# Kernel tuning notes

Measured on AMD Instinct MI355X. Metric: run time of the kernel, lower is better.

## Reference

```python
import jax, jax.numpy as jnp
import numpy as np

H = 16       # num_heads (groups for complex conv)
A = 32       # num frequency anchors
KSZ = 5      # complex conv kernel size
PAD = (KSZ - 1) // 2  # circular padding, matches ComplexConv1DLayer


def setup_inputs() -> dict:
    key = jax.random.key(0)
    ks = jax.random.split(key, 12)
    B, N, D = 4, 2048, 1024
    hid, ghid = 256, 256  # pooling MLP hidden, gate MLP hidden
    F = N // 2 + 1

    def rn(k, shp, s=0.02):
        return jax.random.normal(k, shp, jnp.float32) * s

    return {
        "x": jax.random.normal(ks[0], (B, N, D), jnp.float32),
        "Wv": rn(ks[1], (D, D)), "bv": jnp.zeros((D,), jnp.float32),
        "Wp1": rn(ks[2], (D, hid)), "bp1": jnp.zeros((hid,), jnp.float32),
        "Wp2": rn(ks[3], (hid, 1)), "bp2": jnp.zeros((1,), jnp.float32),
        "Wg1": rn(ks[4], (D, ghid)), "bg1": jnp.zeros((ghid,), jnp.float32),
        "Wg2": rn(ks[5], (ghid, 2 * H * A)), "bg2": jnp.zeros((2 * H * A,), jnp.float32),
        "mod_bias": jnp.zeros((F,), jnp.float32),
        "conv_kr": rn(ks[6], (KSZ,), 1.0 / np.sqrt(KSZ)),
        "conv_ki": rn(ks[7], (KSZ,), 1.0 / np.sqrt(KSZ)),
        "Wo": rn(ks[8], (D, D)), "bo": jnp.zeros((D,), jnp.float32),
    }


def reference(x, Wv, bv, Wp1, bp1, Wp2, bp2, Wg1, bg1, Wg2, bg2,
              mod_bias, conv_kr, conv_ki, Wo, bo):
    B, N, D = x.shape
    dh = D // H
    F = N // 2 + 1

    # value projection -> per-head sequences, rFFT over sequence axis
    v = (x @ Wv + bv).reshape(B, N, H, dh).transpose(0, 2, 1, 3)   # (B,H,N,dh)
    Vf = jnp.fft.rfft(v, axis=2)                                   # (B,H,F,dh) complex64

    # AttentionPoolingLayer: two-layer MLP scores -> softmax over seq -> weighted sum
    s = jax.nn.gelu(x @ Wp1 + bp1, approximate=False) @ Wp2 + bp2  # (B,N,1)
    w = jax.nn.softmax(s, axis=1)
    g = jnp.sum(x * w, axis=1)                                     # (B,D)

    # gate MLP -> complex anchors (B,H,A)
    a = (jax.nn.gelu(g @ Wg1 + bg1, approximate=False) @ Wg2 + bg2).reshape(B, H, A, 2)
    anch_r, anch_i = a[..., 0], a[..., 1]

    # ComplexInterpolationLayer: cubic interpolation of anchors to F bins
    gr = jax.image.resize(anch_r, (B, H, F), method="cubic")
    gi = jax.image.resize(anch_i, (B, H, F), method="cubic")
    gate = gr + 1j * gi                                            # (B,H,F)

    # ComplexModReLULayer: ReLU(|z|+b) * z / |z| with per-frequency bias
    mag = jnp.abs(gate)
    gate = gate * (jax.nn.relu(mag + mod_bias) / (mag + 1e-8))

    # ComplexConv1DLayer: circular-pad complex conv along frequency
    gp = jnp.concatenate([gate[..., -PAD:], gate, gate[..., :PAD]], axis=-1)
    ker = conv_kr.astype(jnp.complex64) + 1j * conv_ki.astype(jnp.complex64)
    gate = sum(ker[j] * gp[..., j:j + F] for j in range(KSZ))      # (B,H,F)

    # spectral gating + inverse FFT + output projection
    y = jnp.fft.irfft(Vf * gate[..., None], n=N, axis=2)           # (B,H,N,dh)
    y = y.transpose(0, 2, 1, 3).reshape(B, N, D)
    return y @ Wo + bo
```

## Files before the change

kernel.cpp:

```cpp
#include <hip/hip_runtime.h>
#include <math.h>

#define NSEQ 2048
#define DMOD 1024
#define NBATCH 4
#define NHEAD 16
#define NFREQ 1025

typedef unsigned short u16t;
typedef __attribute__((ext_vector_type(8))) short short8;
typedef __attribute__((ext_vector_type(4))) float f32x4;

__device__ __forceinline__ float gelu_exact(float x) {
  return 0.5f * x * (1.0f + erff(x * 0.70710678118654752440f));
}
__device__ __forceinline__ u16t bf16_rtn(float x) {
  unsigned u = __float_as_uint(x);
  return (u16t)((u + 0x7FFFu + ((u >> 16) & 1u)) >> 16);
}
__device__ __forceinline__ float bf16f(u16t h) {
  return __uint_as_float(((unsigned)h) << 16);
}
__device__ __forceinline__ void gload_lds16(const u16t* g, u16t* l) {
  __builtin_amdgcn_global_load_lds(
      (const __attribute__((address_space(1))) void*)g,
      (__attribute__((address_space(3))) void*)l, 16, 0, 0);
}

__global__ __launch_bounds__(256) void prep_kernel(
    const float* __restrict__ x, u16t* __restrict__ x_hi, u16t* __restrict__ x_lo,
    const float* __restrict__ Wv, u16t* __restrict__ Tvh, u16t* __restrict__ Tvl,
    const float* __restrict__ Wp1, u16t* __restrict__ Tph, u16t* __restrict__ Tpl) {
  __shared__ float tile[32][33];
  int bx = blockIdx.x;
  int tid = threadIdx.x;
  if (bx < 2048) {
    const int n8 = (NBATCH * NSEQ * DMOD) / 8;
    for (int i = bx * 256 + tid; i < n8; i += 2048 * 256) {
      const float4* p = reinterpret_cast<const float4*>(x + (size_t)i * 8);
      float4 a = p[0], b = p[1];
      float vv[8] = {a.x, a.y, a.z, a.w, b.x, b.y, b.z, b.w};
      alignas(16) u16t th[8];
      alignas(16) u16t tl[8];
#pragma unroll
      for (int e = 0; e < 8; ++e) {
        u16t h = bf16_rtn(vv[e]);
        th[e] = h;
        tl[e] = bf16_rtn(vv[e] - bf16f(h));
      }
      *reinterpret_cast<uint4*>(x_hi + (size_t)i * 8) = *reinterpret_cast<const uint4*>(th);
      *reinterpret_cast<uint4*>(x_lo + (size_t)i * 8) = *reinterpret_cast<const uint4*>(tl);
    }
  } else {
    int idx = bx - 2048;
    int wcol = idx % 40, k0 = (idx / 40) * 32;
    const float* W; u16t* Th; u16t* Tl; int N, n0;
    if (wcol < 32) { W = Wv;  Th = Tvh; Tl = Tvl; N = 1024; n0 = wcol * 32; }
    else           { W = Wp1; Th = Tph; Tl = Tpl; N = 256;  n0 = (wcol - 32) * 32; }
    const int K = 1024;
    int r = tid >> 5, c = tid & 31;
#pragma unroll
    for (int i = 0; i < 4; ++i)
      tile[r + 8 * i][c] = W[(size_t)(k0 + r + 8 * i) * N + n0 + c];
    __syncthreads();
#pragma unroll
    for (int i = 0; i < 4; ++i) {
      int rr = r + 8 * i;
      float v = tile[c][rr];
      u16t h = bf16_rtn(v);
      Th[(size_t)(n0 + rr) * K + k0 + c] = h;
      Tl[(size_t)(n0 + rr) * K + k0 + c] = bf16_rtn(v - bf16f(h));
    }
  }
}

__global__ __launch_bounds__(256) void gemm_fused_kernel(
    const u16t* __restrict__ Ah_g, const u16t* __restrict__ Al_g,
    const u16t* __restrict__ Bvh, const u16t* __restrict__ Bvl,
    const u16t* __restrict__ Bph, const u16t* __restrict__ Bpl,
    const float* __restrict__ bv, const float* __restrict__ bp1,
    const float* __restrict__ Wp2,
    float* __restrict__ vT, float* __restrict__ s_part) {
  __shared__ u16t Ahs[128 * 64], Als[128 * 64], Bhs[128 * 64], Bls[128 * 64];
  __shared__ u16t Php[32 * 64], Ppl[32 * 64];
  const int tid = threadIdx.x;
  const int lane = tid & 63, wave = tid >> 6;
  const int lr = lane & 15, lg = lane >> 4;
  const int wm0 = (wave >> 1) * 64, wn0 = (wave & 1) * 64;
  const int nwg = gridDim.x;
  const int L = (blockIdx.x & 7) * (nwg >> 3) + (blockIdx.x >> 3);
  const int m0 = (L >> 3) * 128;
  const int nblk = L & 7;
  const int n0 = nblk * 128;
  const int pc0 = nblk * 32;
  const int K = 1024;

  f32x4 acc[4][4];
#pragma unroll
  for (int i = 0; i < 4; ++i)
#pragma unroll
    for (int j = 0; j < 4; ++j) acc[i][j] = 0.0f;
  f32x4 accp[2][2];
#pragma unroll
  for (int i = 0; i < 2; ++i)
#pragma unroll
    for (int j = 0; j < 2; ++j) accp[i][j] = 0.0f;

  for (int k0 = 0; k0 < K; k0 += 64) {
#pragma unroll
    for (int q = 0; q < 4; ++q) {
      int cid = q * 256 + tid;
      int row = cid >> 3, grp = cid & 7;
      int koff = k0 + ((grp ^ (row & 7)) << 3);
      size_t ea = (size_t)(m0 + row) * K + koff;
      size_t eb = (size_t)(n0 + row) * K + koff;
      int lbase = q * 2048 + wave * 512;
      gload_lds16(Ah_g + ea, Ahs + lbase);
      gload_lds16(Al_g + ea, Als + lbase);
      gload_lds16(Bvh + eb, Bhs + lbase);
      gload_lds16(Bvl + eb, Bls + lbase);
    }
    {
      int row = tid >> 3, grp = tid & 7;
      int koff = k0 + ((grp ^ (row & 7)) << 3);
      size_t ep = (size_t)(pc0 + row) * K + koff;
      int lbase = wave * 512;
      gload_lds16(Bph + ep, Php + lbase);
      gload_lds16(Bpl + ep, Ppl + lbase);
    }
    __syncthreads();
#pragma unroll
    for (int kf = 0; kf < 2; ++kf) {
      short8 ah[4], al[4];
#pragma unroll
      for (int mi = 0; mi < 4; ++mi) {
        int r_ = wm0 + mi * 16 + lr;
        int g = (kf * 4 + lg) ^ (r_ & 7);
        ah[mi] = *reinterpret_cast<const short8*>(&Ahs[r_ * 64 + g * 8]);
        al[mi] = *reinterpret_cast<const short8*>(&Als[r_ * 64 + g * 8]);
      }
#pragma unroll
      for (int ni = 0; ni < 4; ++ni) {
        int r_ = wn0 + ni * 16 + lr;
        int g = (kf * 4 + lg) ^ (r_ & 7);
        short8 bh8 = *reinterpret_cast<const short8*>(&Bhs[r_ * 64 + g * 8]);
        short8 bl8 = *reinterpret_cast<const short8*>(&Bls[r_ * 64 + g * 8]);
#pragma unroll
        for (int mi = 0; mi < 4; ++mi) {
          acc[mi][ni] = __builtin_amdgcn_mfma_f32_16x16x32_bf16(ah[mi], bh8, acc[mi][ni], 0, 0, 0);
          acc[mi][ni] = __builtin_amdgcn_mfma_f32_16x16x32_bf16(ah[mi], bl8, acc[mi][ni], 0, 0, 0);
          acc[mi][ni] = __builtin_amdgcn_mfma_f32_16x16x32_bf16(al[mi], bh8, acc[mi][ni], 0, 0, 0);
        }
      }
      short8 pah[2], pal[2];
#pragma unroll
      for (int mi = 0; mi < 2; ++mi) {
        int r_ = wave * 32 + mi * 16 + lr;
        int g = (kf * 4 + lg) ^ (r_ & 7);
        pah[mi] = *reinterpret_cast<const short8*>(&Ahs[r_ * 64 + g * 8]);
        pal[mi] = *reinterpret_cast<const short8*>(&Als[r_ * 64 + g * 8]);
      }
#pragma unroll
      for (int ni = 0; ni < 2; ++ni) {
        int r_ = ni * 16 + lr;
        int g = (kf * 4 + lg) ^ (r_ & 7);
        short8 pbh = *reinterpret_cast<const short8*>(&Php[r_ * 64 + g * 8]);
        short8 pbl = *reinterpret_cast<const short8*>(&Ppl[r_ * 64 + g * 8]);
#pragma unroll
        for (int mi = 0; mi < 2; ++mi) {
          accp[mi][ni] = __builtin_amdgcn_mfma_f32_16x16x32_bf16(pah[mi], pbh, accp[mi][ni], 0, 0, 0);
          accp[mi][ni] = __builtin_amdgcn_mfma_f32_16x16x32_bf16(pah[mi], pbl, accp[mi][ni], 0, 0, 0);
          accp[mi][ni] = __builtin_amdgcn_mfma_f32_16x16x32_bf16(pal[mi], pbh, accp[mi][ni], 0, 0, 0);
        }
      }
    }
    __syncthreads();
  }
#pragma unroll
  for (int mi = 0; mi < 4; ++mi)
#pragma unroll
    for (int ni = 0; ni < 4; ++ni) {
      int col = n0 + wn0 + ni * 16 + lr;
      float bvv = bv[col];
      f32x4 a = acc[mi][ni];
      int mbase = m0 + wm0 + mi * 16 + lg * 4;
      int b = mbase >> 11, ss = mbase & 2047;
      float4 o4;
      o4.x = a[0] + bvv; o4.y = a[1] + bvv; o4.z = a[2] + bvv; o4.w = a[3] + bvv;
      *reinterpret_cast<float4*>(vT + (size_t)b * (DMOD * NSEQ) + (size_t)col * NSEQ + ss) = o4;
    }
  {
    float w2[2], bcol[2];
#pragma unroll
    for (int ni = 0; ni < 2; ++ni) {
      int col = pc0 + ni * 16 + lr;
      w2[ni] = Wp2[col];
      bcol[ni] = bp1[col];
    }
#pragma unroll
    for (int mi = 0; mi < 2; ++mi)
#pragma unroll
      for (int r = 0; r < 4; ++r) {
        float p = 0.f;
#pragma unroll
        for (int ni = 0; ni < 2; ++ni)
          p = fmaf(gelu_exact(accp[mi][ni][r] + bcol[ni]), w2[ni], p);
        p += __shfl_xor(p, 1);
        p += __shfl_xor(p, 2);
        p += __shfl_xor(p, 4);
        p += __shfl_xor(p, 8);
        if (lr == 0) {
          int row = m0 + wave * 32 + mi * 16 + lg * 4 + r;
          s_part[nblk * 8192 + row] = p;
        }
      }
  }
}

template<int NBLK>
__global__ __launch_bounds__(256) void mfma_gemm(
    const u16t* __restrict__ Ah_g, const u16t* __restrict__ Al_g,
    const u16t* __restrict__ Bh_g, const u16t* __restrict__ Bl_g,
    const float* __restrict__ bias,
    float* __restrict__ Cf,
    int N, int K) {
  __shared__ u16t Ahs[128 * 64], Als[128 * 64], Bhs[128 * 64], Bls[128 * 64];
  const int tid = threadIdx.x;
  const int lane = tid & 63, wave = tid >> 6;
  const int lr = lane & 15, lg = lane >> 4;
  const int wm0 = (wave >> 1) * 64, wn0 = (wave & 1) * 64;
  const int nwg = gridDim.x;
  const int L = (blockIdx.x & 7) * (nwg >> 3) + (blockIdx.x >> 3);
  const int m0 = (L / NBLK) * 128, n0 = (L % NBLK) * 128;

  f32x4 acc[4][4];
#pragma unroll
  for (int i = 0; i < 4; ++i)
#pragma unroll
    for (int j = 0; j < 4; ++j) acc[i][j] = 0.0f;

  for (int k0 = 0; k0 < K; k0 += 64) {
#pragma unroll
    for (int q = 0; q < 4; ++q) {
      int cid = q * 256 + tid;
      int row = cid >> 3, grp = cid & 7;
      int koff = k0 + ((grp ^ (row & 7)) << 3);
      size_t ea = (size_t)(m0 + row) * K + koff;
      size_t eb = (size_t)(n0 + row) * K + koff;
      int lbase = q * 2048 + wave * 512;
      gload_lds16(Ah_g + ea, Ahs + lbase);
      gload_lds16(Al_g + ea, Als + lbase);
      gload_lds16(Bh_g + eb, Bhs + lbase);
      gload_lds16(Bl_g + eb, Bls + lbase);
    }
    __syncthreads();
#pragma unroll
    for (int kf = 0; kf < 2; ++kf) {
      short8 ah[4], al[4];
#pragma unroll
      for (int mi = 0; mi < 4; ++mi) {
        int r_ = wm0 + mi * 16 + lr;
        int g = (kf * 4 + lg) ^ (r_ & 7);
        ah[mi] = *reinterpret_cast<const short8*>(&Ahs[r_ * 64 + g * 8]);
        al[mi] = *reinterpret_cast<const short8*>(&Als[r_ * 64 + g * 8]);
      }
#pragma unroll
      for (int ni = 0; ni < 4; ++ni) {
        int r_ = wn0 + ni * 16 + lr;
        int g = (kf * 4 + lg) ^ (r_ & 7);
        short8 bh8 = *reinterpret_cast<const short8*>(&Bhs[r_ * 64 + g * 8]);
        short8 bl8 = *reinterpret_cast<const short8*>(&Bls[r_ * 64 + g * 8]);
#pragma unroll
        for (int mi = 0; mi < 4; ++mi) {
          acc[mi][ni] = __builtin_amdgcn_mfma_f32_16x16x32_bf16(ah[mi], bh8, acc[mi][ni], 0, 0, 0);
          acc[mi][ni] = __builtin_amdgcn_mfma_f32_16x16x32_bf16(ah[mi], bl8, acc[mi][ni], 0, 0, 0);
          acc[mi][ni] = __builtin_amdgcn_mfma_f32_16x16x32_bf16(al[mi], bh8, acc[mi][ni], 0, 0, 0);
        }
      }
    }
    __syncthreads();
  }
#pragma unroll
  for (int mi = 0; mi < 4; ++mi)
#pragma unroll
    for (int ni = 0; ni < 4; ++ni) {
      int col = n0 + wn0 + ni * 16 + lr;
      float bvv = bias[col];
      f32x4 a = acc[mi][ni];
#pragma unroll
      for (int r = 0; r < 4; ++r) {
        int row = m0 + wm0 + mi * 16 + lg * 4 + r;
        Cf[(size_t)row * N + col] = a[r] + bvv;
      }
    }
}

#define PADI(i) ((i) + ((i) >> 5))
#define ZSTRIDE 1057

template<int HJ, int TWS>
__device__ __forceinline__ void fwd_reg_stage(float* vr, float* vi,
    const float* TWr, const float* TWi, int lane) {
  float twr_[HJ], twi_[HJ];
#pragma unroll
  for (int t = 0; t < HJ; ++t) {
    int m = (t * 64 + lane) * TWS;
    twr_[t] = TWr[PADI(m)]; twi_[t] = TWi[PADI(m)];
  }
#pragma unroll
  for (int j = 0; j < 16; ++j) {
    if (j & HJ) continue;
    int t = j & (HJ - 1);
    float ur = vr[j], ui = vi[j];
    float wr = vr[j + HJ], wi = vi[j + HJ];
    float dr = ur - wr, di = ui - wi;
    vr[j] = ur + wr; vi[j] = ui + wi;
    vr[j + HJ] = dr * twr_[t] - di * twi_[t];
    vi[j + HJ] = dr * twi_[t] + di * twr_[t];
  }
}

template<int S, int TWS>
__device__ __forceinline__ void fwd_lane_stage(float* vr, float* vi,
    const float* TWr, const float* TWi, int lane) {
  float twr_ = 1.0f, twi_ = 0.0f;
  if (S > 1) {
    int m = (lane & (S - 1)) * TWS;
    twr_ = TWr[PADI(m)]; twi_ = TWi[PADI(m)];
  }
  bool hi = (lane & S) != 0;
#pragma unroll
  for (int j = 0; j < 16; ++j) {
    float or_ = __shfl_xor(vr[j], S, 64);
    float oi_ = __shfl_xor(vi[j], S, 64);
    float sr = vr[j] + or_, si_ = vi[j] + oi_;
    float dr = or_ - vr[j], di = oi_ - vi[j];
    float rr = dr * twr_ - di * twi_;
    float ri = dr * twi_ + di * twr_;
    vr[j] = hi ? rr : sr;
    vi[j] = hi ? ri : si_;
  }
}

template<int S, int TWS>
__device__ __forceinline__ void inv_lane_stage(float* vr, float* vi,
    const float* TWr, const float* TWi, int lane) {
  float twr_ = 1.0f, twi_ = 0.0f;
  if (S > 1) {
    int m = (lane & (S - 1)) * TWS;
    twr_ = TWr[PADI(m)]; twi_ = -TWi[PADI(m)];
  }
  bool hi = (lane & S) != 0;
#pragma unroll
  for (int j = 0; j < 16; ++j) {
    float xr = vr[j], xi = vi[j];
    if (S > 1) {
      float pr = xr * twr_ - xi * twi_;
      float pi = xr * twi_ + xi * twr_;
      xr = hi ? pr : xr;
      xi = hi ? pi : xi;
    }
    float or_ = __shfl_xor(xr, S, 64);
    float oi_ = __shfl_xor(xi, S, 64);
    vr[j] = hi ? (or_ - xr) : (xr + or_);
    vi[j] = hi ? (oi_ - xi) : (xi + oi_);
  }
}

template<int HJ, int TWS>
__device__ __forceinline__ void inv_reg_stage(float* vr, float* vi,
    const float* TWr, const float* TWi, int lane) {
  float twr_[HJ], twi_[HJ];
#pragma unroll
  for (int t = 0; t < HJ; ++t) {
    int m = (t * 64 + lane) * TWS;
    twr_[t] = TWr[PADI(m)]; twi_[t] = -TWi[PADI(m)];
  }
#pragma unroll
  for (int j = 0; j < 16; ++j) {
    if (j & HJ) continue;
    int t = j & (HJ - 1);
    float ur = vr[j], ui = vi[j];
    float br = vr[j + HJ], bi = vi[j + HJ];
    float wr = br * twr_[t] - bi * twi_[t];
    float wi = br * twi_[t] + bi * twr_[t];
    vr[j] = ur + wr; vi[j] = ui + wi;
    vr[j + HJ] = ur - wr; vi[j + HJ] = ui - wi;
  }
}

__global__ __launch_bounds__(1024) void conv_fft_kernel(
    const float* __restrict__ vT, const float* __restrict__ gateb,
    u16t* __restrict__ yh, u16t* __restrict__ yl) {
  __shared__ float Zr[16 * ZSTRIDE], Zi[16 * ZSTRIDE];
  __shared__ float TWr[528], TWi[528];
  const int tid = threadIdx.x;
  const int lane = tid & 63, wave = tid >> 6;
  const int c0 = blockIdx.x * 16;
  const int b = blockIdx.y;
  const int bh = b * NHEAD + (c0 >> 6);
  const float* gate_bh = gateb + (size_t)bh * NFREQ * 2;

  if (tid < 512) {
    float si, co;
    sincosf(-3.14159265358979323846f * (float)tid * (1.0f / 512.0f), &si, &co);
    TWr[PADI(tid)] = co; TWi[PADI(tid)] = si;
  }
  __syncthreads();

  float* zr = Zr + wave * ZSTRIDE;
  float* zi = Zi + wave * ZSTRIDE;
  const float* col = vT + ((size_t)b * DMOD + (c0 + wave)) * NSEQ;

  float vr[16], vi[16];
#pragma unroll
  for (int j = 0; j < 16; ++j) {
    float2 w2 = *reinterpret_cast<const float2*>(col + 2 * (j * 64 + lane));
    vr[j] = w2.x; vi[j] = w2.y;
  }

  fwd_reg_stage<8, 1>(vr, vi, TWr, TWi, lane);
  fwd_reg_stage<4, 2>(vr, vi, TWr, TWi, lane);
  fwd_reg_stage<2, 4>(vr, vi, TWr, TWi, lane);
  fwd_reg_stage<1, 8>(vr, vi, TWr, TWi, lane);
  fwd_lane_stage<32, 16>(vr, vi, TWr, TWi, lane);
  fwd_lane_stage<16, 32>(vr, vi, TWr, TWi, lane);
  fwd_lane_stage<8, 64>(vr, vi, TWr, TWi, lane);
  fwd_lane_stage<4, 128>(vr, vi, TWr, TWi, lane);
  fwd_lane_stage<2, 256>(vr, vi, TWr, TWi, lane);
  fwd_lane_stage<1, 0>(vr, vi, TWr, TWi, lane);

#pragma unroll
  for (int j = 0; j < 16; ++j) {
    int p = PADI(j * 64 + lane);
    zr[p] = vr[j]; zi[p] = vi[j];
  }
  asm volatile("s_waitcnt lgkmcnt(0)" ::: "memory");

  const float s1 = 1.0f / 1024.0f;
#pragma unroll
  for (int q = 0; q < 8; ++q) {
    int k = q * 64 + lane;
    if (k == 0) {
      float z0r = zr[0], z0i = zi[0];
      float X0 = z0r + z0i;
      float XN = z0r - z0i;
      float2 G0 = *reinterpret_cast<const float2*>(gate_bh + 0);
      float2 GN = *reinterpret_cast<const float2*>(gate_bh + 1024 * 2);
      float y0 = X0 * G0.x * s1;
      float yN = XN * GN.x * s1;
      zr[0] = 0.5f * (y0 + yN); zi[0] = 0.5f * (y0 - yN);
      float zmr = zr[1], zmi = zi[1];
      float X5r = zmr, X5i = -zmi;
      float2 G5 = *reinterpret_cast<const float2*>(gate_bh + 512 * 2);
      float Y5r = (X5r * G5.x - X5i * G5.y) * s1;
      float Y5i = (X5r * G5.y + X5i * G5.x) * s1;
      zr[1] = Y5r; zi[1] = -Y5i;
    } else {
      int kq = 1024 - k;
      int rp = PADI((int)(__brev((unsigned)k) >> 22));
      int rq = PADI((int)(__brev((unsigned)kq) >> 22));
      float Zkr = zr[rp], Zki = zi[rp];
      float Zqr = zr[rq], Zqi = zi[rq];
      float Er = 0.5f * (Zkr + Zqr), Ei = 0.5f * (Zki - Zqi);
      float Odr = 0.5f * (Zki + Zqi), Odi = -0.5f * (Zkr - Zqr);
      float ti, tr;
      sincosf(-3.14159265358979323846f * (float)k * (1.0f / 1024.0f), &ti, &tr);
      float Pr = Odr * tr - Odi * ti, Pi = Odr * ti + Odi * tr;
      float Xkr = Er + Pr, Xki = Ei + Pi;
      float Xqr = Er - Pr, Xqi = -(Ei - Pi);
      float2 Gk = *reinterpret_cast<const float2*>(gate_bh + k * 2);
      float2 Gq = *reinterpret_cast<const float2*>(gate_bh + kq * 2);
      float Ykr = (Xkr * Gk.x - Xki * Gk.y) * s1;
      float Yki = (Xkr * Gk.y + Xki * Gk.x) * s1;
      float Yqr = (Xqr * Gq.x - Xqi * Gq.y) * s1;
      float Yqi = (Xqr * Gq.y + Xqi * Gq.x) * s1;
      float E2r = 0.5f * (Ykr + Yqr), E2i = 0.5f * (Yki - Yqi);
      float D2r = 0.5f * (Ykr - Yqr), D2i = 0.5f * (Yki + Yqi);
      float O2r = D2r * tr + D2i * ti, O2i = D2i * tr - D2r * ti;
      zr[rp] = E2r - O2i; zi[rp] = E2i + O2r;
      zr[rq] = E2r + O2i; zi[rq] = O2r - E2i;
    }
  }
  asm volatile("s_waitcnt lgkmcnt(0)" ::: "memory");

#pragma unroll
  for (int j = 0; j < 16; ++j) {
    int p = PADI(j * 64 + lane);
    vr[j] = zr[p]; vi[j] = zi[p];
  }
  asm volatile("s_waitcnt lgkmcnt(0)" ::: "memory");

  inv_lane_stage<1, 0>(vr, vi, TWr, TWi, lane);
  inv_lane_stage<2, 256>(vr, vi, TWr, TWi, lane);
  inv_lane_stage<4, 128>(vr, vi, TWr, TWi, lane);
  inv_lane_stage<8, 64>(vr, vi, TWr, TWi, lane);
  inv_lane_stage<16, 32>(vr, vi, TWr, TWi, lane);
  inv_lane_stage<32, 16>(vr, vi, TWr, TWi, lane);
  inv_reg_stage<1, 8>(vr, vi, TWr, TWi, lane);
  inv_reg_stage<2, 4>(vr, vi, TWr, TWi, lane);
  inv_reg_stage<4, 2>(vr, vi, TWr, TWi, lane);
  inv_reg_stage<8, 1>(vr, vi, TWr, TWi, lane);

#pragma unroll
  for (int j = 0; j < 16; ++j) {
    int p = PADI(j * 64 + lane);
    zr[p] = vr[j]; zi[p] = vi[j];
  }
  __syncthreads();

  {
    alignas(16) u16t he[16], le[16], ho[16], lo_[16];
    int p = PADI(tid);
#pragma unroll
    for (int w = 0; w < 16; ++w) {
      float re = Zr[w * ZSTRIDE + p];
      float im = Zi[w * ZSTRIDE + p];
      u16t hr = bf16_rtn(re);
      he[w] = hr; le[w] = bf16_rtn(re - bf16f(hr));
      u16t hm = bf16_rtn(im);
      ho[w] = hm; lo_[w] = bf16_rtn(im - bf16f(hm));
    }
    size_t o0 = ((size_t)b * NSEQ + 2 * tid) * DMOD + c0;
    size_t o1 = o0 + DMOD;
    *reinterpret_cast<uint4*>(yh + o0) = reinterpret_cast<const uint4*>(he)[0];
    *reinterpret_cast<uint4*>(yh + o0 + 8) = reinterpret_cast<const uint4*>(he)[1];
    *reinterpret_cast<uint4*>(yl + o0) = reinterpret_cast<const uint4*>(le)[0];
    *reinterpret_cast<uint4*>(yl + o0 + 8) = reinterpret_cast<const uint4*>(le)[1];
    *reinterpret_cast<uint4*>(yh + o1) = reinterpret_cast<const uint4*>(ho)[0];
    *reinterpret_cast<uint4*>(yh + o1 + 8) = reinterpret_cast<const uint4*>(ho)[1];
    *reinterpret_cast<uint4*>(yl + o1) = reinterpret_cast<const uint4*>(lo_)[0];
    *reinterpret_cast<uint4*>(yl + o1 + 8) = reinterpret_cast<const uint4*>(lo_)[1];
  }
}

__global__ __launch_bounds__(256) void wo_pool_kernel(
    const float* __restrict__ Wo, u16t* __restrict__ Toh, u16t* __restrict__ Tol,
    const float* __restrict__ x, const float* __restrict__ s_part,
    const float* __restrict__ bp2, float* __restrict__ gpart) {
  __shared__ float tile[32][33];
  __shared__ float red[256];
  __shared__ float wsh[128];
  int bx = blockIdx.x;
  int tid = threadIdx.x;
  if (bx < 1024) {
    int n0 = (bx & 31) * 32, k0 = (bx >> 5) * 32;
    int r = tid >> 5, c = tid & 31;
#pragma unroll
    for (int i = 0; i < 4; ++i)
      tile[r + 8 * i][c] = Wo[(size_t)(k0 + r + 8 * i) * 1024 + n0 + c];
    __syncthreads();
#pragma unroll
    for (int i = 0; i < 4; ++i) {
      int rr = r + 8 * i;
      float v = tile[c][rr];
      u16t h = bf16_rtn(v);
      Toh[(size_t)(n0 + rr) * 1024 + k0 + c] = h;
      Tol[(size_t)(n0 + rr) * 1024 + k0 + c] = bf16_rtn(v - bf16f(h));
    }
  } else {
    int idx = bx - 1024;
    int chunk = idx & 15, b = idx >> 4;
    float bp = bp2[0];
    float sv[8];
    float m = -1e30f;
#pragma unroll
    for (int q = 0; q < 8; ++q) {
      int row = b * NSEQ + q * 256 + tid;
      float v = bp;
#pragma unroll
      for (int c = 0; c < 8; ++c) v += s_part[c * 8192 + row];
      sv[q] = v;
      m = fmaxf(m, v);
    }
    red[tid] = m; __syncthreads();
    for (int o = 128; o; o >>= 1) { if (tid < o) red[tid] = fmaxf(red[tid], red[tid + o]); __syncthreads(); }
    float bm = red[0]; __syncthreads();
    float sum = 0.f;
#pragma unroll
    for (int q = 0; q < 8; ++q) sum += expf(sv[q] - bm);
    red[tid] = sum; __syncthreads();
    for (int o = 128; o; o >>= 1) { if (tid < o) red[tid] += red[tid + o]; __syncthreads(); }
    float inv = 1.0f / red[0];
    __syncthreads();
    int n0 = chunk * 128;
    if (tid < 128) {
      int row = b * NSEQ + n0 + tid;
      float v = bp;
#pragma unroll
      for (int c = 0; c < 8; ++c) v += s_part[c * 8192 + row];
      wsh[tid] = expf(v - bm) * inv;
    }
    __syncthreads();
    float acc[4] = {};
    for (int n = 0; n < 128; ++n) {
      float wn = wsh[n];
      const float* xr = &x[((size_t)b * NSEQ + n0 + n) * DMOD];
#pragma unroll
      for (int q = 0; q < 4; ++q) acc[q] = fmaf(wn, xr[tid + 256 * q], acc[q]);
    }
    float* gp = &gpart[((size_t)b * 16 + chunk) * DMOD];
#pragma unroll
    for (int q = 0; q < 4; ++q) gp[tid + 256 * q] = acc[q];
  }
}

__device__ __forceinline__ float keys_cubic(float x) {
  if (x >= 2.0f) return 0.0f;
  if (x >= 1.0f) return ((-0.5f * x + 2.5f) * x - 4.0f) * x + 2.0f;
  return ((1.5f * x - 2.5f) * x) * x + 1.0f;
}

__global__ __launch_bounds__(256) void gate_kernel(
    const float* __restrict__ gpart, const float* __restrict__ Wg1,
    const float* __restrict__ bg1,
    const float* __restrict__ Wg2, const float* __restrict__ bg2,
    const float* __restrict__ mod_bias,
    const float* __restrict__ kr5, const float* __restrict__ ki5,
    float* __restrict__ gate_out) {
  int bh = blockIdx.x;
  int tid = threadIdx.x;
  __shared__ float g_s[1024];
  __shared__ float hs_s[256];
  __shared__ float anch_s[64];
  __shared__ float ar_[32], ai_[32];
  __shared__ float gr[NFREQ], gi[NFREQ];
  int b = bh >> 4, h = bh & 15;
  for (int d = tid; d < 1024; d += 256) {
    float acc = 0.f;
#pragma unroll
    for (int j = 0; j < 16; ++j)
      acc += gpart[((size_t)b * 16 + j) * DMOD + d];
    g_s[d] = acc;
  }
  __syncthreads();
  {
    float a0 = 0.f, a1 = 0.f, a2 = 0.f, a3 = 0.f;
    for (int i = 0; i < 1024; i += 4) {
      a0 = fmaf(g_s[i], Wg1[(size_t)i * 256 + tid], a0);
      a1 = fmaf(g_s[i + 1], Wg1[(size_t)(i + 1) * 256 + tid], a1);
      a2 = fmaf(g_s[i + 2], Wg1[(size_t)(i + 2) * 256 + tid], a2);
      a3 = fmaf(g_s[i + 3], Wg1[(size_t)(i + 3) * 256 + tid], a3);
    }
    hs_s[tid] = gelu_exact(bg1[tid] + ((a0 + a1) + (a2 + a3)));
  }
  __syncthreads();
  if (tid < 64) {
    int cc = h * 64 + tid;
    float a2 = bg2[cc];
    for (int i = 0; i < 256; ++i) a2 = fmaf(hs_s[i], Wg2[(size_t)i * 1024 + cc], a2);
    anch_s[tid] = a2;
  }
  __syncthreads();
  if (tid < 32) {
    ar_[tid] = anch_s[tid * 2 + 0];
    ai_[tid] = anch_s[tid * 2 + 1];
  }
  __syncthreads();
  const float inv_scale = 32.0f / 1025.0f;
  for (int f = tid; f < NFREQ; f += 256) {
    float c = (f + 0.5f) * inv_scale - 0.5f;
    int j0 = (int)floorf(c) - 1;
    float wr = 0.f, wi = 0.f, wsum = 0.f;
#pragma unroll
    for (int u = 0; u < 4; ++u) {
      int j = j0 + u;
      if (j < 0 || j > 31) continue;
      float w = keys_cubic(fabsf(c - (float)j));
      wsum += w;
      wr = fmaf(w, ar_[j], wr);
      wi = fmaf(w, ai_[j], wi);
    }
    float invw = 1.0f / wsum;
    wr *= invw; wi *= invw;
    float mag = sqrtf(wr * wr + wi * wi);
    float scale = fmaxf(mag + mod_bias[f], 0.0f) / (mag + 1e-8f);
    gr[f] = wr * scale;
    gi[f] = wi * scale;
  }
  __syncthreads();
  float k_r[5], k_i[5];
#pragma unroll
  for (int j = 0; j < 5; ++j) { k_r[j] = kr5[j]; k_i[j] = ki5[j]; }
  for (int f = tid; f < NFREQ; f += 256) {
    float cr = 0.f, ci = 0.f;
#pragma unroll
    for (int j = 0; j < 5; ++j) {
      int idx = f + j - 2;
      if (idx < 0) idx += NFREQ;
      else if (idx >= NFREQ) idx -= NFREQ;
      float a = gr[idx], bb = gi[idx];
      cr = fmaf(k_r[j], a, cr); cr = fmaf(-k_i[j], bb, cr);
      ci = fmaf(k_r[j], bb, ci); ci = fmaf(k_i[j], a, ci);
    }
    gate_out[((size_t)bh * NFREQ + f) * 2 + 0] = cr;
    gate_out[((size_t)bh * NFREQ + f) * 2 + 1] = ci;
  }
}

extern "C" void kernel_launch(void* const* d_in, const int* in_sizes, int n_in,
                              void* d_out, int out_size, void* d_ws, size_t ws_size,
                              hipStream_t stream) {
  const float* x        = (const float*)d_in[0];
  const float* Wv       = (const float*)d_in[1];
  const float* bv       = (const float*)d_in[2];
  const float* Wp1      = (const float*)d_in[3];
  const float* bp1      = (const float*)d_in[4];
  const float* Wp2      = (const float*)d_in[5];
  const float* bp2      = (const float*)d_in[6];
  const float* Wg1      = (const float*)d_in[7];
  const float* bg1      = (const float*)d_in[8];
  const float* Wg2      = (const float*)d_in[9];
  const float* bg2      = (const float*)d_in[10];
  const float* mod_bias = (const float*)d_in[11];
  const float* ckr      = (const float*)d_in[12];
  const float* cki      = (const float*)d_in[13];
  const float* Wo       = (const float*)d_in[14];
  const float* bo       = (const float*)d_in[15];

  const int M = NBATCH * NSEQ;
  const size_t MD = (size_t)M * DMOD;
  char* wsb = (char*)d_ws;

  u16t* x_hi = (u16t*)wsb;
  u16t* x_lo = x_hi + MD;
  u16t* y_hi = x_hi;
  u16t* y_lo = x_lo;
  u16t* WT_h = (u16t*)(wsb + (size_t)32 * 1024 * 1024);
  u16t* WT_l = (u16t*)(wsb + (size_t)34 * 1024 * 1024);
  u16t* WTp1_h = (u16t*)(wsb + (size_t)36 * 1024 * 1024);
  u16t* WTp1_l = (u16t*)(wsb + (size_t)36 * 1024 * 1024 + 524288);
  float* s_part = (float*)(wsb + (size_t)37 * 1024 * 1024);
  float* gpart = (float*)(wsb + (size_t)36 * 1024 * 1024);
  float* gateb = gpart + 65536;

  float* vT  = (float*)d_out;
  float* out = (float*)d_out;

  dim3 blk(256);

  prep_kernel<<<dim3(2048 + 1280), blk, 0, stream>>>(
      x, x_hi, x_lo, Wv, WT_h, WT_l, Wp1, WTp1_h, WTp1_l);
  gemm_fused_kernel<<<dim3(512), blk, 0, stream>>>(
      x_hi, x_lo, WT_h, WT_l, WTp1_h, WTp1_l, bv, bp1, Wp2, vT, s_part);
  wo_pool_kernel<<<dim3(1024 + 64), blk, 0, stream>>>(
      Wo, WT_h, WT_l, x, s_part, bp2, gpart);
  gate_kernel<<<dim3(NBATCH * NHEAD), blk, 0, stream>>>(
      gpart, Wg1, bg1, Wg2, bg2, mod_bias, ckr, cki, gateb);
  conv_fft_kernel<<<dim3(DMOD / 16, NBATCH), dim3(1024), 0, stream>>>(
      vT, gateb, y_hi, y_lo);
  mfma_gemm<8><<<dim3((DMOD / 128) * (M / 128)), blk, 0, stream>>>(
      y_hi, y_lo, WT_h, WT_l, bo, out, DMOD, 1024);
}
```

Baseline: 231.5 us.

## Shrink FFT blocks to 4 columns and move bf16 split/transpose to separate kernel

The spectral conv FFT kernel now uses 256-thread blocks handling 4 channels instead of 1024-thread blocks handling 16. Its large 135KB shared buffer shrinks, so more blocks can reside per CU. The inverse-FFT result is written in place to the fp32 buffer. A new tiled transpose kernel then reads it back and produces the hi/lo bf16 split in token-major layout. This trades better occupancy for an extra kernel launch and an extra full read/write of the 32MB intermediate through global memory.

```diff
diff --git a/kernel.cpp b/kernel.cpp
--- a/kernel.cpp
+++ b/kernel.cpp
@@ -296,7 +296,6 @@
 }
 
 #define PADI(i) ((i) + ((i) >> 5))
-#define ZSTRIDE 1057
 
 template<int HJ, int TWS>
 __device__ __forceinline__ void fwd_reg_stage(float* vr, float* vi,
@@ -389,28 +388,29 @@
   }
 }
 
-__global__ __launch_bounds__(1024) void conv_fft_kernel(
-    const float* __restrict__ vT, const float* __restrict__ gateb,
-    u16t* __restrict__ yh, u16t* __restrict__ yl) {
-  __shared__ float Zr[16 * ZSTRIDE], Zi[16 * ZSTRIDE];
+__global__ __launch_bounds__(256) void conv_fft_kernel(
+    float* __restrict__ vio, const float* __restrict__ gateb) {
+  __shared__ float Zr[4][1056], Zi[4][1056];
   __shared__ float TWr[528], TWi[528];
   const int tid = threadIdx.x;
   const int lane = tid & 63, wave = tid >> 6;
-  const int c0 = blockIdx.x * 16;
+  const int c0 = blockIdx.x * 4;
   const int b = blockIdx.y;
   const int bh = b * NHEAD + (c0 >> 6);
   const float* gate_bh = gateb + (size_t)bh * NFREQ * 2;
 
-  if (tid < 512) {
+#pragma unroll
+  for (int q = 0; q < 2; ++q) {
+    int m = q * 256 + tid;
     float si, co;
-    sincosf(-3.14159265358979323846f * (float)tid * (1.0f / 512.0f), &si, &co);
-    TWr[PADI(tid)] = co; TWi[PADI(tid)] = si;
+    sincosf(-3.14159265358979323846f * (float)m * (1.0f / 512.0f), &si, &co);
+    TWr[PADI(m)] = co; TWi[PADI(m)] = si;
   }
   __syncthreads();
 
-  float* zr = Zr + wave * ZSTRIDE;
-  float* zi = Zi + wave * ZSTRIDE;
-  const float* col = vT + ((size_t)b * DMOD + (c0 + wave)) * NSEQ;
+  float* zr = Zr[wave];
+  float* zi = Zi[wave];
+  float* col = vio + ((size_t)b * DMOD + (c0 + wave)) * NSEQ;
 
   float vr[16], vi[16];
 #pragma unroll
@@ -504,33 +504,39 @@
 
 #pragma unroll
   for (int j = 0; j < 16; ++j) {
-    int p = PADI(j * 64 + lane);
-    zr[p] = vr[j]; zi[p] = vi[j];
+    *reinterpret_cast<float2*>(col + 2 * (j * 64 + lane)) = make_float2(vr[j], vi[j]);
+  }
+}
+
+__global__ __launch_bounds__(256) void tysplit_kernel(
+    const float* __restrict__ yT, u16t* __restrict__ yh, u16t* __restrict__ yl) {
+  __shared__ float tile[64][65];
+  int t0 = blockIdx.x * 64, c0 = blockIdx.y * 64, b = blockIdx.z;
+  int r = threadIdx.x >> 4;
+  int cc = (threadIdx.x & 15) * 4;
+#pragma unroll
+  for (int i = 0; i < 4; ++i) {
+    int row = r + 16 * i;
+    float4 w = *reinterpret_cast<const float4*>(
+        yT + ((size_t)b * DMOD + c0 + row) * NSEQ + t0 + cc);
+    tile[row][cc] = w.x; tile[row][cc + 1] = w.y;
+    tile[row][cc + 2] = w.z; tile[row][cc + 3] = w.w;
   }
   __syncthreads();
-
-  {
-    alignas(16) u16t he[16], le[16], ho[16], lo_[16];
-    int p = PADI(tid);
-#pragma unroll
-    for (int w = 0; w < 16; ++w) {
-      float re = Zr[w * ZSTRIDE + p];
-      float im = Zi[w * ZSTRIDE + p];
-      u16t hr = bf16_rtn(re);
-      he[w] = hr; le[w] = bf16_rtn(re - bf16f(hr));
-      u16t hm = bf16_rtn(im);
-      ho[w] = hm; lo_[w] = bf16_rtn(im - bf16f(hm));
-    }
-    size_t o0 = ((size_t)b * NSEQ + 2 * tid) * DMOD + c0;
-    size_t o1 = o0 + DMOD;
-    *reinterpret_cast<uint4*>(yh + o0) = reinterpret_cast<const uint4*>(he)[0];
-    *reinterpret_cast<uint4*>(yh + o0 + 8) = reinterpret_cast<const uint4*>(he)[1];
-    *reinterpret_cast<uint4*>(yl + o0) = reinterpret_cast<const uint4*>(le)[0];
-    *reinterpret_cast<uint4*>(yl + o0 + 8) = reinterpret_cast<const uint4*>(le)[1];
-    *reinterpret_cast<uint4*>(yh + o1) = reinterpret_cast<const uint4*>(ho)[0];
-    *reinterpret_cast<uint4*>(yh + o1 + 8) = reinterpret_cast<const uint4*>(ho)[1];
-    *reinterpret_cast<uint4*>(yl + o1) = reinterpret_cast<const uint4*>(lo_)[0];
-    *reinterpret_cast<uint4*>(yl + o1 + 8) = reinterpret_cast<const uint4*>(lo_)[1];
+#pragma unroll
+  for (int i = 0; i < 4; ++i) {
+    int tt = r + 16 * i;
+    alignas(8) u16t hh[4], ll[4];
+#pragma unroll
+    for (int e = 0; e < 4; ++e) {
+      float v = tile[cc + e][tt];
+      u16t h = bf16_rtn(v);
+      hh[e] = h;
+      ll[e] = bf16_rtn(v - bf16f(h));
+    }
+    size_t o = ((size_t)b * NSEQ + t0 + tt) * DMOD + c0 + cc;
+    *reinterpret_cast<ushort4*>(yh + o) = *reinterpret_cast<const ushort4*>(hh);
+    *reinterpret_cast<ushort4*>(yl + o) = *reinterpret_cast<const ushort4*>(ll);
   }
 }
 
@@ -747,8 +753,8 @@
       Wo, WT_h, WT_l, x, s_part, bp2, gpart);
   gate_kernel<<<dim3(NBATCH * NHEAD), blk, 0, stream>>>(
       gpart, Wg1, bg1, Wg2, bg2, mod_bias, ckr, cki, gateb);
-  conv_fft_kernel<<<dim3(DMOD / 16, NBATCH), dim3(1024), 0, stream>>>(
-      vT, gateb, y_hi, y_lo);
+  conv_fft_kernel<<<dim3(DMOD / 4, NBATCH), blk, 0, stream>>>(vT, gateb);
+  tysplit_kernel<<<dim3(NSEQ / 64, DMOD / 64, NBATCH), blk, 0, stream>>>(vT, y_hi, y_lo);
   mfma_gemm<8><<<dim3((DMOD / 128) * (M / 128)), blk, 0, stream>>>(
       y_hi, y_lo, WT_h, WT_l, bo, out, DMOD, 1024);
 }
```

Result: no change. 234.1 us (+1.1%).
